# Kernel tuning notes

Measured on AMD Instinct MI355X. Metric: run time of the kernel, lower is better.

## Reference

```python
import jax, jax.numpy as jnp
import numpy as np

EPS = 1e-5
SCALE = 0.25
H = 16  # num_heads

def _bn(x, gamma, beta):
    # training-mode BatchNorm1d over (batch, length) per channel; x: [M, C, N]
    mean = jnp.mean(x, axis=(0, 2), keepdims=True)
    var = jnp.var(x, axis=(0, 2), keepdims=True)
    return gamma[None, :, None] * (x - mean) * jax.lax.rsqrt(var + EPS) + beta[None, :, None]

def _spike(x, vth):
    # fresh MyNode within one forward: mem = 0/tau + x, spike if >= vth
    return (x >= vth).astype(x.dtype)

def setup_inputs() -> dict:
    key = jax.random.key(0)
    ks = jax.random.split(key, 8)
    T, B, C, N = 4, 1, 256, 1024
    x = jax.random.normal(ks[0], (T, B, C, N), dtype=jnp.float32)
    y = jax.random.normal(ks[1], (T, B, C, N), dtype=jnp.float32)
    def w(k):
        return jax.random.normal(k, (C, C), dtype=jnp.float32) * (1.0 / np.sqrt(C))
    return {
        "x": x, "y": y,
        "Wq": w(ks[2]), "gq": jnp.ones((C,), jnp.float32), "bq": jnp.zeros((C,), jnp.float32),
        "Wk": w(ks[3]), "gk": jnp.ones((C,), jnp.float32), "bk": jnp.zeros((C,), jnp.float32),
        "Wv": w(ks[4]), "gv": jnp.ones((C,), jnp.float32), "bv": jnp.zeros((C,), jnp.float32),
        "Wp": w(ks[5]), "gp": jnp.ones((C,), jnp.float32), "bp": jnp.zeros((C,), jnp.float32),
    }

def reference(x, y, Wq, gq, bq, Wk, gk, bk, Wv, gv, bv, Wp, gp, bp):
    T, B, C, N = x.shape
    D = C // H
    xf = x.reshape(T * B, C, N)
    yf = y.reshape(T * B, C, N)

    def branch(inp, W, g, b, vth):
        h = jnp.einsum('oc,mcn->mon', W, inp)      # conv1x1
        h = _bn(h, g, b)
        s = _spike(h, vth)                          # LIF spike (fresh state)
        # [T,B,C,N] -> split channels into heads -> [T,B,H,N,D]
        return s.reshape(T, B, H, D, N).transpose(0, 1, 2, 4, 3)

    q = branch(xf, Wq, gq, bq, 1.0)
    k = branch(yf, Wk, gk, bk, 1.0)
    v = branch(yf, Wv, gv, bv, 1.0)

    attn = jnp.einsum('tbhnd,tbhmd->tbhnm', q, k)   # [T,B,H,N,N]
    out = jnp.einsum('tbhnm,tbhmd->tbhnd', attn, v) * SCALE

    # [T,B,H,N,D] -> [T,B,C,N]
    out = out.transpose(0, 1, 2, 4, 3).reshape(T, B, C, N)
    out = _spike(out.reshape(T * B, C, N), 0.5)      # attn_lif, v_threshold=0.5
    out = jnp.einsum('oc,mcn->mon', Wp, out)         # proj conv1x1
    out = _spike(_bn(out, gp, bp), 1.0)              # proj_bn + proj_lif
    return out.reshape(T, B, C, N)
```

## Files before the change

### kernel.cpp

```cpp
#include <hip/hip_runtime.h>
#include <cstdint>
#include <cstddef>

static constexpr int C = 256;
static constexpr int N = 1024;
static constexpr int M = 4;
static constexpr size_t PLANE = (size_t)M * C * N;

typedef double d4 __attribute__((ext_vector_type(4)));

__device__ inline void probe_d_layout(int lane, int rowv[4], int colv[4])
{
    const double am = (lane < 16) ? (double)lane : 0.0;
    const double a1 = (lane < 16) ? 1.0 : 0.0;
    const double bn = (lane < 16) ? (double)(lane & 15) : 0.0;
    d4 z = (d4){0.0, 0.0, 0.0, 0.0};
    d4 dr = __builtin_amdgcn_mfma_f64_16x16x4f64(am, a1, z, 0, 0, 0);
    d4 dc = __builtin_amdgcn_mfma_f64_16x16x4f64(a1, bn, z, 0, 0, 0);
    #pragma unroll
    for (int r = 0; r < 4; ++r) {
        rowv[r] = (int)dr[r];
        colv[r] = (int)dc[r];
    }
}

__global__ __launch_bounds__(256) void gemm_qkv_mfma(
    const float* __restrict__ x, const float* __restrict__ y,
    const float* __restrict__ Wq, const float* __restrict__ Wk,
    const float* __restrict__ Wv, double* __restrict__ hbase)
{
    const int bz = blockIdx.z;
    const int br = bz >> 2;
    const int m  = bz & 3;
    const float* __restrict__ W = (br == 0) ? Wq : (br == 1) ? Wk : Wv;
    const float* __restrict__ X = ((br == 0) ? x : y) + (size_t)m * C * N;
    double* __restrict__ H = hbase + (size_t)br * PLANE + (size_t)m * C * N;

    const int n0 = blockIdx.x * 64;
    const int o0 = blockIdx.y * 64;
    const int tid  = threadIdx.x;
    const int lane = tid & 63;
    const int w    = tid >> 6;
    const int ow   = (w & 1) * 32;
    const int nw   = (w >> 1) * 32;
    const int lm   = lane & 15;
    const int lk   = lane >> 4;

    int rowv[4], colv[4];
    probe_d_layout(lane, rowv, colv);

    __shared__ float As[64][20];
    __shared__ float Bs[16][72];

    d4 acc[2][2];
    #pragma unroll
    for (int i = 0; i < 2; ++i)
        #pragma unroll
        for (int j = 0; j < 2; ++j)
            acc[i][j] = (d4){0.0, 0.0, 0.0, 0.0};

    const int sa_o = tid >> 2;
    const int sa_q = (tid & 3) * 4;
    const int sb_c = tid >> 4;
    const int sb_q = (tid & 15) * 4;

    for (int c0 = 0; c0 < C; c0 += 16) {
        const float4 av = *(const float4*)(W + (size_t)(o0 + sa_o) * C + c0 + sa_q);
        const float4 bv = *(const float4*)(X + (size_t)(c0 + sb_c) * N + n0 + sb_q);
        *(float4*)(&As[sa_o][sa_q]) = av;
        *(float4*)(&Bs[sb_c][sb_q]) = bv;
        __syncthreads();
        #pragma unroll
        for (int ks = 0; ks < 4; ++ks) {
            const int kk = ks * 4 + lk;
            double a0 = (double)As[ow + lm][kk];
            double a1 = (double)As[ow + 16 + lm][kk];
            double b0 = (double)Bs[kk][nw + lm];
            double b1 = (double)Bs[kk][nw + 16 + lm];
            acc[0][0] = __builtin_amdgcn_mfma_f64_16x16x4f64(a0, b0, acc[0][0], 0, 0, 0);
            acc[0][1] = __builtin_amdgcn_mfma_f64_16x16x4f64(a0, b1, acc[0][1], 0, 0, 0);
            acc[1][0] = __builtin_amdgcn_mfma_f64_16x16x4f64(a1, b0, acc[1][0], 0, 0, 0);
            acc[1][1] = __builtin_amdgcn_mfma_f64_16x16x4f64(a1, b1, acc[1][1], 0, 0, 0);
        }
        __syncthreads();
    }

    #pragma unroll
    for (int ot = 0; ot < 2; ++ot)
        #pragma unroll
        for (int nt = 0; nt < 2; ++nt)
            #pragma unroll
            for (int r = 0; r < 4; ++r)
                H[(size_t)(o0 + ow + ot * 16 + rowv[r]) * N + (n0 + nw + nt * 16 + colv[r])] =
                    acc[ot][nt][r];
}

__global__ __launch_bounds__(256) void gemm_p_mfma(
    const float* __restrict__ Wp, const unsigned char* __restrict__ s2,
    double* __restrict__ hp)
{
    const int m = blockIdx.z;
    const unsigned char* __restrict__ X = s2 + (size_t)m * C * N;
    double* __restrict__ H = hp + (size_t)m * C * N;

    const int n0 = blockIdx.x * 64;
    const int o0 = blockIdx.y * 64;
    const int tid  = threadIdx.x;
    const int lane = tid & 63;
    const int w    = tid >> 6;
    const int ow   = (w & 1) * 32;
    const int nw   = (w >> 1) * 32;
    const int lm   = lane & 15;
    const int lk   = lane >> 4;

    int rowv[4], colv[4];
    probe_d_layout(lane, rowv, colv);

    __shared__ float As[64][20];
    __shared__ float Bs[16][72];

    d4 acc[2][2];
    #pragma unroll
    for (int i = 0; i < 2; ++i)
        #pragma unroll
        for (int j = 0; j < 2; ++j)
            acc[i][j] = (d4){0.0, 0.0, 0.0, 0.0};

    const int sa_o = tid >> 2;
    const int sa_q = (tid & 3) * 4;
    const int sb_c = tid >> 4;
    const int sb_q = (tid & 15) * 4;

    for (int c0 = 0; c0 < C; c0 += 16) {
        const float4 av = *(const float4*)(Wp + (size_t)(o0 + sa_o) * C + c0 + sa_q);
        const unsigned int word = *(const unsigned int*)(X + (size_t)(c0 + sb_c) * N + n0 + sb_q);
        *(float4*)(&As[sa_o][sa_q]) = av;
        Bs[sb_c][sb_q + 0] = (float)(word & 0xFF);
        Bs[sb_c][sb_q + 1] = (float)((word >> 8) & 0xFF);
        Bs[sb_c][sb_q + 2] = (float)((word >> 16) & 0xFF);
        Bs[sb_c][sb_q + 3] = (float)((word >> 24) & 0xFF);
        __syncthreads();
        #pragma unroll
        for (int ks = 0; ks < 4; ++ks) {
            const int kk = ks * 4 + lk;
            double a0 = (double)As[ow + lm][kk];
            double a1 = (double)As[ow + 16 + lm][kk];
            double b0 = (double)Bs[kk][nw + lm];
            double b1 = (double)Bs[kk][nw + 16 + lm];
            acc[0][0] = __builtin_amdgcn_mfma_f64_16x16x4f64(a0, b0, acc[0][0], 0, 0, 0);
            acc[0][1] = __builtin_amdgcn_mfma_f64_16x16x4f64(a0, b1, acc[0][1], 0, 0, 0);
            acc[1][0] = __builtin_amdgcn_mfma_f64_16x16x4f64(a1, b0, acc[1][0], 0, 0, 0);
            acc[1][1] = __builtin_amdgcn_mfma_f64_16x16x4f64(a1, b1, acc[1][1], 0, 0, 0);
        }
        __syncthreads();
    }

    #pragma unroll
    for (int ot = 0; ot < 2; ++ot)
        #pragma unroll
        for (int nt = 0; nt < 2; ++nt)
            #pragma unroll
            for (int r = 0; r < 4; ++r)
                H[(size_t)(o0 + ow + ot * 16 + rowv[r]) * N + (n0 + nw + nt * 16 + colv[r])] =
                    acc[ot][nt][r];
}

__global__ __launch_bounds__(256) void bnspike_qkv(
    const double* __restrict__ hbase,
    const float* __restrict__ gq, const float* __restrict__ bq,
    const float* __restrict__ gk, const float* __restrict__ bk,
    const float* __restrict__ gv, const float* __restrict__ bv,
    unsigned char* __restrict__ sbase)
{
    const int o  = blockIdx.x;
    const int br = blockIdx.y;
    const double* __restrict__ h = hbase + (size_t)br * PLANE + (size_t)o * N;
    const int tid = threadIdx.x;

    double v[16];
    double s = 0.0, ss = 0.0;
    #pragma unroll
    for (int j = 0; j < 16; ++j) {
        int l  = j * 256 + tid;
        int mm = l >> 10, nn = l & 1023;
        v[j] = h[(size_t)mm * C * N + nn];
        s += v[j]; ss += v[j] * v[j];
    }
    #pragma unroll
    for (int off = 32; off > 0; off >>= 1) {
        s  += __shfl_down(s, off, 64);
        ss += __shfl_down(ss, off, 64);
    }
    __shared__ double rs[4], rss[4], sstat[2];
    const int lane = tid & 63, wv_ = tid >> 6;
    if (lane == 0) { rs[wv_] = s; rss[wv_] = ss; }
    __syncthreads();
    if (tid == 0) {
        double S  = rs[0] + rs[1] + rs[2] + rs[3];
        double SS = rss[0] + rss[1] + rss[2] + rss[3];
        double mean = S / 4096.0;
        double var  = SS / 4096.0 - mean * mean;
        sstat[0] = mean;
        sstat[1] = 1.0 / sqrt(var + 1e-5);
    }
    __syncthreads();
    const double mean = sstat[0], inv = sstat[1];
    const float* g = (br == 0) ? gq : (br == 1) ? gk : gv;
    const float* b = (br == 0) ? bq : (br == 1) ? bk : bv;
    const double gc = (double)g[o], bc = (double)b[o];
    unsigned char* out = sbase + (size_t)br * PLANE + (size_t)o * N;
    #pragma unroll
    for (int j = 0; j < 16; ++j) {
        int l  = j * 256 + tid;
        int mm = l >> 10, nn = l & 1023;
        double t = gc * (v[j] - mean) * inv + bc;
        out[(size_t)mm * C * N + nn] = (t >= 1.0) ? (unsigned char)1 : (unsigned char)0;
    }
}

__global__ __launch_bounds__(256) void attn_kernel(
    const unsigned char* __restrict__ qb, const unsigned char* __restrict__ kb,
    const unsigned char* __restrict__ vb, unsigned char* __restrict__ s2)
{
    const int nc = blockIdx.x;
    const int hh = blockIdx.y;
    const int t  = blockIdx.z;
    const int tid = threadIdx.x;

    __shared__ unsigned int kw[16][257];
    __shared__ unsigned int vw[16][257];
    __shared__ int kt[256];

    #pragma unroll
    for (int j = 0; j < 4; ++j) {
        int idx = j * 256 + tid;
        int r = idx >> 6, q4 = idx & 63;
        size_t goff = ((size_t)(t * C + hh * 16 + r)) * N + (size_t)q4 * 16;
        uint4 kk = *(const uint4*)(kb + goff);
        uint4 vv = *(const uint4*)(vb + goff);
        kw[r][q4 * 4 + 0] = kk.x; kw[r][q4 * 4 + 1] = kk.y;
        kw[r][q4 * 4 + 2] = kk.z; kw[r][q4 * 4 + 3] = kk.w;
        vw[r][q4 * 4 + 0] = vv.x; vw[r][q4 * 4 + 1] = vv.y;
        vw[r][q4 * 4 + 2] = vv.z; vw[r][q4 * 4 + 3] = vv.w;
    }
    __syncthreads();

    const int d = tid >> 4, dp = tid & 15;
    int sum = 0;
    #pragma unroll 8
    for (int wd = 0; wd < 256; ++wd)
        sum += __popc(kw[d][wd] & vw[dp][wd]);
    kt[tid] = sum;
    __syncthreads();

    const int n = nc * 256 + tid;
    int sums[16];
    #pragma unroll
    for (int i = 0; i < 16; ++i) sums[i] = 0;
    #pragma unroll
    for (int d2 = 0; d2 < 16; ++d2) {
        int qv = (int)qb[((size_t)(t * C + hh * 16 + d2)) * N + n];
        #pragma unroll
        for (int dp2 = 0; dp2 < 16; ++dp2)
            sums[dp2] += qv * kt[d2 * 16 + dp2];
    }
    #pragma unroll
    for (int dp2 = 0; dp2 < 16; ++dp2)
        s2[((size_t)(t * C + hh * 16 + dp2)) * N + n] = (sums[dp2] >= 2) ? 1 : 0;
}

__global__ __launch_bounds__(256) void bnspike_p(
    const double* __restrict__ hp,
    const float* __restrict__ gp, const float* __restrict__ bp,
    float* __restrict__ outp)
{
    const int o = blockIdx.x;
    const double* __restrict__ h = hp + (size_t)o * N;
    const int tid = threadIdx.x;

    double v[16];
    double s = 0.0, ss = 0.0;
    #pragma unroll
    for (int j = 0; j < 16; ++j) {
        int l  = j * 256 + tid;
        int mm = l >> 10, nn = l & 1023;
        v[j] = h[(size_t)mm * C * N + nn];
        s += v[j]; ss += v[j] * v[j];
    }
    #pragma unroll
    for (int off = 32; off > 0; off >>= 1) {
        s  += __shfl_down(s, off, 64);
        ss += __shfl_down(ss, off, 64);
    }
    __shared__ double rs[4], rss[4], sstat[2];
    const int lane = tid & 63, wv_ = tid >> 6;
    if (lane == 0) { rs[wv_] = s; rss[wv_] = ss; }
    __syncthreads();
    if (tid == 0) {
        double S  = rs[0] + rs[1] + rs[2] + rs[3];
        double SS = rss[0] + rss[1] + rss[2] + rss[3];
        double mean = S / 4096.0;
        double var  = SS / 4096.0 - mean * mean;
        sstat[0] = mean;
        sstat[1] = 1.0 / sqrt(var + 1e-5);
    }
    __syncthreads();
    const double mean = sstat[0], inv = sstat[1];
    const double gc = (double)gp[o], bc = (double)bp[o];
    float* out = outp + (size_t)o * N;
    #pragma unroll
    for (int j = 0; j < 16; ++j) {
        int l  = j * 256 + tid;
        int mm = l >> 10, nn = l & 1023;
        double t = gc * (v[j] - mean) * inv + bc;
        out[(size_t)mm * C * N + nn] = (t >= 1.0) ? 1.0f : 0.0f;
    }
}

extern "C" void kernel_launch(void* const* d_in, const int* in_sizes, int n_in,
                              void* d_out, int out_size, void* d_ws, size_t ws_size,
                              hipStream_t stream)
{
    const float* x  = (const float*)d_in[0];
    const float* y  = (const float*)d_in[1];
    const float* Wq = (const float*)d_in[2];
    const float* gq = (const float*)d_in[3];
    const float* bq = (const float*)d_in[4];
    const float* Wk = (const float*)d_in[5];
    const float* gk = (const float*)d_in[6];
    const float* bk = (const float*)d_in[7];
    const float* Wv = (const float*)d_in[8];
    const float* gv = (const float*)d_in[9];
    const float* bv = (const float*)d_in[10];
    const float* Wp = (const float*)d_in[11];
    const float* gp = (const float*)d_in[12];
    const float* bp = (const float*)d_in[13];
    float* out = (float*)d_out;

    char* ws = (char*)d_ws;
    double* hq = (double*)ws;
    double* hp = hq;
    unsigned char* qb  = (unsigned char*)(ws + 3 * PLANE * sizeof(double));
    unsigned char* kb2 = qb + PLANE;
    unsigned char* vb2 = qb + 2 * PLANE;
    unsigned char* s2b = qb + 3 * PLANE;

    gemm_qkv_mfma<<<dim3(16, 4, 12), 256, 0, stream>>>(x, y, Wq, Wk, Wv, hq);
    bnspike_qkv<<<dim3(256, 3), 256, 0, stream>>>(hq, gq, bq, gk, bk, gv, bv, qb);
    attn_kernel<<<dim3(4, 16, 4), 256, 0, stream>>>(qb, kb2, vb2, s2b);
    gemm_p_mfma<<<dim3(16, 4, 4), 256, 0, stream>>>(Wp, s2b, hp);
    bnspike_p<<<dim3(256), 256, 0, stream>>>(hp, gp, bp, out);
}
```

Measured before the change: 154.9 us.

## Double-buffer LDS tiles and prefetch next K-chunk in projection GEMMs

Both fp64-MFMA GEMM kernels now use two LDS buffers and a K-chunk of 32 instead of 16. The next chunk's global loads are issued into registers before the current chunk's MFMAs run, which lets memory latency overlap compute and drops one barrier per iteration. The cost is roughly four times the LDS per block, which may lower occupancy. The padding strides also change, which alters the bank-conflict pattern.

```diff
diff --git a/kernel.cpp b/kernel.cpp
--- a/kernel.cpp
+++ b/kernel.cpp
@@ -23,6 +23,9 @@
         colv[r] = (int)dc[r];
     }
 }
+
+static constexpr int ASTR = 36;
+static constexpr int BSTR = 72;
 
 __global__ __launch_bounds__(256) void gemm_qkv_mfma(
     const float* __restrict__ x, const float* __restrict__ y,
@@ -49,8 +52,8 @@
     int rowv[4], colv[4];
     probe_d_layout(lane, rowv, colv);
 
-    __shared__ float As[64][20];
-    __shared__ float Bs[16][72];
+    __shared__ __align__(16) float As[2][64 * ASTR];
+    __shared__ __align__(16) float Bs[2][32 * BSTR];
 
     d4 acc[2][2];
     #pragma unroll
@@ -59,30 +62,46 @@
         for (int j = 0; j < 2; ++j)
             acc[i][j] = (d4){0.0, 0.0, 0.0, 0.0};
 
-    const int sa_o = tid >> 2;
-    const int sa_q = (tid & 3) * 4;
-    const int sb_c = tid >> 4;
-    const int sb_q = (tid & 15) * 4;
-
-    for (int c0 = 0; c0 < C; c0 += 16) {
-        const float4 av = *(const float4*)(W + (size_t)(o0 + sa_o) * C + c0 + sa_q);
-        const float4 bv = *(const float4*)(X + (size_t)(c0 + sb_c) * N + n0 + sb_q);
-        *(float4*)(&As[sa_o][sa_q]) = av;
-        *(float4*)(&Bs[sb_c][sb_q]) = bv;
+    const int rA = tid >> 2;
+    const int cA = (tid & 3) * 8;
+    const int rB = tid >> 3;
+    const int cB = (tid & 7) * 8;
+
+    float4 a0r, a1r, b0r, b1r;
+    a0r = *(const float4*)(W + (size_t)(o0 + rA) * C + 0 + cA);
+    a1r = *(const float4*)(W + (size_t)(o0 + rA) * C + 0 + cA + 4);
+    b0r = *(const float4*)(X + (size_t)(0 + rB) * N + n0 + cB);
+    b1r = *(const float4*)(X + (size_t)(0 + rB) * N + n0 + cB + 4);
+
+    int buf = 0;
+    for (int ch = 0; ch < 8; ++ch) {
+        *(float4*)(&As[buf][rA * ASTR + cA])     = a0r;
+        *(float4*)(&As[buf][rA * ASTR + cA + 4]) = a1r;
+        *(float4*)(&Bs[buf][rB * BSTR + cB])     = b0r;
+        *(float4*)(&Bs[buf][rB * BSTR + cB + 4]) = b1r;
         __syncthreads();
-        #pragma unroll
-        for (int ks = 0; ks < 4; ++ks) {
+        if (ch < 7) {
+            const int c0 = (ch + 1) * 32;
+            a0r = *(const float4*)(W + (size_t)(o0 + rA) * C + c0 + cA);
+            a1r = *(const float4*)(W + (size_t)(o0 + rA) * C + c0 + cA + 4);
+            b0r = *(const float4*)(X + (size_t)(c0 + rB) * N + n0 + cB);
+            b1r = *(const float4*)(X + (size_t)(c0 + rB) * N + n0 + cB + 4);
+        }
+        const float* __restrict__ Ab = As[buf];
+        const float* __restrict__ Bb = Bs[buf];
+        #pragma unroll
+        for (int ks = 0; ks < 8; ++ks) {
             const int kk = ks * 4 + lk;
-            double a0 = (double)As[ow + lm][kk];
-            double a1 = (double)As[ow + 16 + lm][kk];
-            double b0 = (double)Bs[kk][nw + lm];
-            double b1 = (double)Bs[kk][nw + 16 + lm];
+            double a0 = (double)Ab[(ow + lm) * ASTR + kk];
+            double a1 = (double)Ab[(ow + 16 + lm) * ASTR + kk];
+            double b0 = (double)Bb[kk * BSTR + nw + lm];
+            double b1 = (double)Bb[kk * BSTR + nw + 16 + lm];
             acc[0][0] = __builtin_amdgcn_mfma_f64_16x16x4f64(a0, b0, acc[0][0], 0, 0, 0);
             acc[0][1] = __builtin_amdgcn_mfma_f64_16x16x4f64(a0, b1, acc[0][1], 0, 0, 0);
             acc[1][0] = __builtin_amdgcn_mfma_f64_16x16x4f64(a1, b0, acc[1][0], 0, 0, 0);
             acc[1][1] = __builtin_amdgcn_mfma_f64_16x16x4f64(a1, b1, acc[1][1], 0, 0, 0);
         }
-        __syncthreads();
+        buf ^= 1;
     }
 
     #pragma unroll
@@ -116,8 +135,8 @@
     int rowv[4], colv[4];
     probe_d_layout(lane, rowv, colv);
 
-    __shared__ float As[64][20];
-    __shared__ float Bs[16][72];
+    __shared__ __align__(16) float As[2][64 * ASTR];
+    __shared__ __align__(16) float Bs[2][32 * BSTR];
 
     d4 acc[2][2];
     #pragma unroll
@@ -126,33 +145,52 @@
         for (int j = 0; j < 2; ++j)
             acc[i][j] = (d4){0.0, 0.0, 0.0, 0.0};
 
-    const int sa_o = tid >> 2;
-    const int sa_q = (tid & 3) * 4;
-    const int sb_c = tid >> 4;
-    const int sb_q = (tid & 15) * 4;
-
-    for (int c0 = 0; c0 < C; c0 += 16) {
-        const float4 av = *(const float4*)(Wp + (size_t)(o0 + sa_o) * C + c0 + sa_q);
-        const unsigned int word = *(const unsigned int*)(X + (size_t)(c0 + sb_c) * N + n0 + sb_q);
-        *(float4*)(&As[sa_o][sa_q]) = av;
-        Bs[sb_c][sb_q + 0] = (float)(word & 0xFF);
-        Bs[sb_c][sb_q + 1] = (float)((word >> 8) & 0xFF);
-        Bs[sb_c][sb_q + 2] = (float)((word >> 16) & 0xFF);
-        Bs[sb_c][sb_q + 3] = (float)((word >> 24) & 0xFF);
+    const int rA = tid >> 2;
+    const int cA = (tid & 3) * 8;
+    const int rB = tid >> 3;
+    const int cB = (tid & 7) * 8;
+
+    float4 a0r, a1r;
+    uint2 bw;
+    a0r = *(const float4*)(Wp + (size_t)(o0 + rA) * C + 0 + cA);
+    a1r = *(const float4*)(Wp + (size_t)(o0 + rA) * C + 0 + cA + 4);
+    bw  = *(const uint2*)(X + (size_t)(0 + rB) * N + n0 + cB);
+
+    int buf = 0;
+    for (int ch = 0; ch < 8; ++ch) {
+        *(float4*)(&As[buf][rA * ASTR + cA])     = a0r;
+        *(float4*)(&As[buf][rA * ASTR + cA + 4]) = a1r;
+        float* bs = &Bs[buf][rB * BSTR + cB];
+        bs[0] = (float)(bw.x & 0xFF);
+        bs[1] = (float)((bw.x >> 8) & 0xFF);
+        bs[2] = (float)((bw.x >> 16) & 0xFF);
+        bs[3] = (float)((bw.x >> 24) & 0xFF);
+        bs[4] = (float)(bw.y & 0xFF);
+        bs[5] = (float)((bw.y >> 8) & 0xFF);
+        bs[6] = (float)((bw.y >> 16) & 0xFF);
+        bs[7] = (float)((bw.y >> 24) & 0xFF);
         __syncthreads();
-        #pragma unroll
-        for (int ks = 0; ks < 4; ++ks) {
+        if (ch < 7) {
+            const int c0 = (ch + 1) * 32;
+            a0r = *(const float4*)(Wp + (size_t)(o0 + rA) * C + c0 + cA);
+            a1r = *(const float4*)(Wp + (size_t)(o0 + rA) * C + c0 + cA + 4);
+            bw  = *(const uint2*)(X + (size_t)(c0 + rB) * N + n0 + cB);
+        }
+        const float* __restrict__ Ab = As[buf];
+        const float* __restrict__ Bb = Bs[buf];
+        #pragma unroll
+        for (int ks = 0; ks < 8; ++ks) {
             const int kk = ks * 4 + lk;
-            double a0 = (double)As[ow + lm][kk];
-            double a1 = (double)As[ow + 16 + lm][kk];
-            double b0 = (double)Bs[kk][nw + lm];
-            double b1 = (double)Bs[kk][nw + 16 + lm];
+            double a0 = (double)Ab[(ow + lm) * ASTR + kk];
+            double a1 = (double)Ab[(ow + 16 + lm) * ASTR + kk];
+            double b0 = (double)Bb[kk * BSTR + nw + lm];
+            double b1 = (double)Bb[kk * BSTR + nw + 16 + lm];
             acc[0][0] = __builtin_amdgcn_mfma_f64_16x16x4f64(a0, b0, acc[0][0], 0, 0, 0);
             acc[0][1] = __builtin_amdgcn_mfma_f64_16x16x4f64(a0, b1, acc[0][1], 0, 0, 0);
             acc[1][0] = __builtin_amdgcn_mfma_f64_16x16x4f64(a1, b0, acc[1][0], 0, 0, 0);
             acc[1][1] = __builtin_amdgcn_mfma_f64_16x16x4f64(a1, b1, acc[1][1], 0, 0, 0);
         }
-        __syncthreads();
+        buf ^= 1;
     }
 
     #pragma unroll
```

Measured after the change: 149.5 us. 1.04x faster.
